# Kernel tuning notes

Measured on AMD Instinct MI355X. Metric: run time of the kernel, lower is better.

The kernel has to match this reference:

```python
import jax, jax.numpy as jnp
import numpy as np
import math

B, T, D = 4, 2048, 1024
H, DH = 16, 64  # n_heads, d_head; H*DH == D


def setup_inputs() -> dict:
    key = jax.random.key(0)
    ks = jax.random.split(key, 5)
    s = 0.02
    return {
        "x": jax.random.normal(ks[0], (B, T, D), dtype=jnp.float32),
        "W_qkv": jax.random.normal(ks[1], (D, 3 * D), dtype=jnp.float32) * s,
        "b_qkv": jnp.zeros((3 * D,), dtype=jnp.float32),
        "W_out": jax.random.normal(ks[2], (D, D), dtype=jnp.float32) * s,
        "b_out": jnp.zeros((D,), dtype=jnp.float32),
    }


def reference(x, W_qkv, b_qkv, W_out, b_out):
    Bx, Tx, Cx = x.shape
    qkv = x @ W_qkv + b_qkv                      # [B,T,3D]
    q, k, v = jnp.split(qkv, 3, axis=-1)
    q = q.reshape(Bx, Tx, H, DH).transpose(0, 2, 1, 3)  # [B,H,T,dh]
    k = k.reshape(Bx, Tx, H, DH).transpose(0, 2, 1, 3)
    v = v.reshape(Bx, Tx, H, DH).transpose(0, 2, 1, 3)
    scores = jnp.einsum("bhqd,bhkd->bhqk", q, k) / math.sqrt(DH)
    causal = jnp.tril(jnp.ones((Tx, Tx), dtype=bool))
    scores = jnp.where(causal, scores, jnp.float32(-jnp.inf))
    attn = jax.nn.softmax(scores, axis=-1)       # dropout p=0.0 -> identity
    out = jnp.einsum("bhqk,bhkd->bhqd", attn, v)
    out = out.transpose(0, 2, 1, 3).reshape(Bx, Tx, Cx)
    return out @ W_out + b_out
```

## Files before the change

### kernel.cpp

```cpp
#include <hip/hip_runtime.h>

#define DEVI __device__ __forceinline__

typedef __attribute__((ext_vector_type(8))) short short8;
typedef __attribute__((ext_vector_type(4))) float floatx4;

typedef const __attribute__((address_space(1))) void* gbl_ptr_t;
typedef __attribute__((address_space(3))) void* lds_ptr_t;

DEVI unsigned short f2bf(float f) {
  union { float f; unsigned int u; } v; v.f = f;
  unsigned int r = v.u + 0x7fffu + ((v.u >> 16) & 1u);
  return (unsigned short)(r >> 16);
}

DEVI float redsum16(float v) {
  v += __shfl_xor(v, 1);
  v += __shfl_xor(v, 2);
  v += __shfl_xor(v, 4);
  v += __shfl_xor(v, 8);
  return v;
}

constexpr int Bc = 4, Tc = 2048, Dc = 1024, Hc = 16, DHc = 64;
constexpr int Mrows = Bc * Tc;
constexpr long PLANE = (long)Bc * Hc * Tc * DHc;

__global__ __launch_bounds__(256) void cast_f32_bf16(const float* __restrict__ in,
                                                     unsigned short* __restrict__ out, int n4) {
  int i = blockIdx.x * 256 + threadIdx.x;
  if (i < n4) {
    float4 v = ((const float4*)in)[i];
    ushort4 o;
    o.x = f2bf(v.x); o.y = f2bf(v.y); o.z = f2bf(v.z); o.w = f2bf(v.w);
    ((ushort4*)out)[i] = o;
  }
}

__global__ __launch_bounds__(256) void transpose_cast(const float* __restrict__ in,
                                                      unsigned short* __restrict__ out,
                                                      int K, int N) {
  __shared__ float tile[32][33];
  int bx = blockIdx.x * 32;
  int by = blockIdx.y * 32;
  int tx = threadIdx.x & 31, ty = threadIdx.x >> 5;
#pragma unroll
  for (int i = ty; i < 32; i += 8) tile[i][tx] = in[(long)(by + i) * N + bx + tx];
  __syncthreads();
#pragma unroll
  for (int i = ty; i < 32; i += 8) out[(long)(bx + i) * K + by + tx] = f2bf(tile[tx][i]);
}

template <int MODE>
__global__ __launch_bounds__(256) void gemm_bt(const unsigned short* __restrict__ A,
                                               const unsigned short* __restrict__ Bt,
                                               const float* __restrict__ bias,
                                               void* __restrict__ Cout,
                                               int M, int N, int K) {
  constexpr int BK = 64;
  __shared__ __align__(16) short As[128 * 64];
  __shared__ __align__(16) short Bs[128 * 64];

  const int tid = threadIdx.x;
  const int wave = tid >> 6;
  const int lane = tid & 63;
  const int l16 = lane & 15;
  const int quad = lane >> 4;
  const int wm = (wave >> 1) * 64;
  const int wn = (wave & 1) * 64;
  const int rsub = lane >> 3;
  const int csub = (lane & 7) * 8;

  const long row0 = (long)blockIdx.y * 128;
  const long col0 = (long)blockIdx.x * 128;

  floatx4 acc[4][4];
#pragma unroll
  for (int i = 0; i < 4; i++)
#pragma unroll
    for (int j = 0; j < 4; j++) acc[i][j] = (floatx4){0.f, 0.f, 0.f, 0.f};

  for (int k0 = 0; k0 < K; k0 += BK) {
#pragma unroll
    for (int c = 0; c < 4; c++) {
      int rb = (c * 4 + wave) * 8;
      const unsigned short* sA = &A[(row0 + rb + rsub) * (long)K + k0 + csub];
      __builtin_amdgcn_global_load_lds((gbl_ptr_t)sA, (lds_ptr_t)&As[rb * 64], 16, 0, 0);
      const unsigned short* sB = &Bt[(col0 + rb + rsub) * (long)K + k0 + csub];
      __builtin_amdgcn_global_load_lds((gbl_ptr_t)sB, (lds_ptr_t)&Bs[rb * 64], 16, 0, 0);
    }
    __syncthreads();
#pragma unroll
    for (int kk = 0; kk < BK; kk += 32) {
      short8 af[4], bfr[4];
#pragma unroll
      for (int mt = 0; mt < 4; mt++)
        af[mt] = *(const short8*)&As[(wm + mt * 16 + l16) * 64 + kk + quad * 8];
#pragma unroll
      for (int nt = 0; nt < 4; nt++)
        bfr[nt] = *(const short8*)&Bs[(wn + nt * 16 + l16) * 64 + kk + quad * 8];
#pragma unroll
      for (int mt = 0; mt < 4; mt++)
#pragma unroll
        for (int nt = 0; nt < 4; nt++)
          acc[mt][nt] = __builtin_amdgcn_mfma_f32_16x16x32_bf16(af[mt], bfr[nt], acc[mt][nt], 0, 0, 0);
    }
    __syncthreads();
  }

#pragma unroll
  for (int mt = 0; mt < 4; mt++)
#pragma unroll
    for (int nt = 0; nt < 4; nt++)
#pragma unroll
      for (int r = 0; r < 4; r++) {
        long row = row0 + wm + mt * 16 + quad * 4 + r;
        long col = col0 + wn + nt * 16 + l16;
        float v = acc[mt][nt][r] + bias[col];
        if (MODE == 0) {
          int which = (int)(col >> 10);
          int hc = (int)col & 1023;
          int h = hc >> 6, d = hc & 63;
          int b = (int)(row >> 11), t = (int)row & 2047;
          ((unsigned short*)Cout)[(long)which * PLANE +
                                  (((long)(b * Hc + h) * Tc + t) << 6) + d] = f2bf(v);
        } else {
          ((float*)Cout)[row * N + col] = v;
        }
      }
}

__global__ __launch_bounds__(256) void flash_attn(const unsigned short* __restrict__ qkv,
                                                  unsigned short* __restrict__ attn_out) {
  constexpr int PD = 72;
  __shared__ __align__(16) short Ks[64 * PD];
  __shared__ __align__(16) short Vts[64 * PD];
  __shared__ __align__(16) short Ps[4 * 16 * PD];

  const int tid = threadIdx.x;
  const int wave = tid >> 6;
  const int lane = tid & 63;
  const int l16 = lane & 15;
  const int quad = lane >> 4;

  const int bh = blockIdx.y;
  const long base = (long)bh * Tc * DHc;
  const unsigned short* Qg = qkv + base;
  const unsigned short* Kg = qkv + PLANE + base;
  const unsigned short* Vg = qkv + 2 * PLANE + base;
  const int b = bh >> 4, h = bh & 15;

  constexpr float CEXP = 0.125f * 1.44269504f;
  short* Pw = &Ps[wave * 16 * PD];

  const int kr = tid >> 3;
  const int kc = (tid & 7) * 8;

#pragma unroll 1
  for (int pass = 0; pass < 2; pass++) {
    const int qx = (pass == 0) ? (int)blockIdx.x : (31 - (int)blockIdx.x);
    const int q0 = qx * 64 + wave * 16;

    short8 qf[2];
#pragma unroll
    for (int kk = 0; kk < 2; kk++)
      qf[kk] = *(const short8*)&Qg[(long)(q0 + l16) * 64 + kk * 32 + quad * 8];

    floatx4 oacc[4];
#pragma unroll
    for (int j = 0; j < 4; j++) oacc[j] = (floatx4){0.f, 0.f, 0.f, 0.f};
    float lpart[4] = {0.f, 0.f, 0.f, 0.f};

    const int ntiles = qx + 1;

    uint4 Kreg[2], Vreg[2];
    Kreg[0] = *(const uint4*)&Kg[(long)kr * 64 + kc];
    Kreg[1] = *(const uint4*)&Kg[(long)(32 + kr) * 64 + kc];
    Vreg[0] = *(const uint4*)&Vg[(long)lane * 64 + wave * 8];
    Vreg[1] = *(const uint4*)&Vg[(long)lane * 64 + (wave + 4) * 8];

#pragma unroll 1
    for (int kt = 0; kt < ntiles; kt++) {
      __syncthreads();
      *(uint4*)&Ks[kr * PD + kc] = Kreg[0];
      *(uint4*)&Ks[(32 + kr) * PD + kc] = Kreg[1];
#pragma unroll
      for (int c = 0; c < 2; c++) {
        int dc = wave + 4 * c;
        unsigned short vb[8];
        *(uint4*)vb = Vreg[c];
#pragma unroll
        for (int j = 0; j < 8; j++) Vts[(dc * 8 + j) * PD + lane] = (short)vb[j];
      }
      __syncthreads();
      if (kt + 1 < ntiles) {
        long koff = (long)(kt + 1) * 64;
        Kreg[0] = *(const uint4*)&Kg[(koff + kr) * 64 + kc];
        Kreg[1] = *(const uint4*)&Kg[(koff + 32 + kr) * 64 + kc];
        Vreg[0] = *(const uint4*)&Vg[(koff + lane) * 64 + wave * 8];
        Vreg[1] = *(const uint4*)&Vg[(koff + lane) * 64 + (wave + 4) * 8];
      }

      floatx4 sacc[4];
#pragma unroll
      for (int j = 0; j < 4; j++) sacc[j] = (floatx4){0.f, 0.f, 0.f, 0.f};
#pragma unroll
      for (int kk = 0; kk < 2; kk++) {
        short8 kf[4];
#pragma unroll
        for (int nt = 0; nt < 4; nt++)
          kf[nt] = *(const short8*)&Ks[(nt * 16 + l16) * PD + kk * 32 + quad * 8];
#pragma unroll
        for (int nt = 0; nt < 4; nt++)
          sacc[nt] = __builtin_amdgcn_mfma_f32_16x16x32_bf16(qf[kk], kf[nt], sacc[nt], 0, 0, 0);
      }

      if (kt == qx) {
#pragma unroll
        for (int nt = 0; nt < 4; nt++) {
          int ki = kt * 64 + nt * 16 + l16;
#pragma unroll
          for (int r = 0; r < 4; r++) {
            int qi = q0 + quad * 4 + r;
            if (ki > qi) sacc[nt][r] = -3.0e38f;
          }
        }
      }

#pragma unroll
      for (int nt = 0; nt < 4; nt++)
#pragma unroll
        for (int r = 0; r < 4; r++) sacc[nt][r] = exp2f(sacc[nt][r] * CEXP);
#pragma unroll
      for (int r = 0; r < 4; r++)
        lpart[r] += (sacc[0][r] + sacc[1][r]) + (sacc[2][r] + sacc[3][r]);

#pragma unroll
      for (int nt = 0; nt < 4; nt++)
#pragma unroll
        for (int r = 0; r < 4; r++)
          Pw[(quad * 4 + r) * PD + nt * 16 + l16] = (short)f2bf(sacc[nt][r]);

#pragma unroll
      for (int kk = 0; kk < 2; kk++) {
        short8 pf = *(const short8*)&Pw[l16 * PD + kk * 32 + quad * 8];
        short8 vf[4];
#pragma unroll
        for (int dt = 0; dt < 4; dt++)
          vf[dt] = *(const short8*)&Vts[(dt * 16 + l16) * PD + kk * 32 + quad * 8];
#pragma unroll
        for (int dt = 0; dt < 4; dt++)
          oacc[dt] = __builtin_amdgcn_mfma_f32_16x16x32_bf16(pf, vf[dt], oacc[dt], 0, 0, 0);
      }
    }

#pragma unroll
    for (int r = 0; r < 4; r++) {
      float l = redsum16(lpart[r]);
      float inv = 1.0f / l;
      int t = q0 + quad * 4 + r;
#pragma unroll
      for (int dt = 0; dt < 4; dt++) {
        int d = dt * 16 + l16;
        attn_out[(((long)(b * Tc + t) * Hc + h) << 6) + d] = f2bf(oacc[dt][r] * inv);
      }
    }
  }
}

extern "C" void kernel_launch(void* const* d_in, const int* in_sizes, int n_in,
                              void* d_out, int out_size, void* d_ws, size_t ws_size,
                              hipStream_t stream) {
  const float* x = (const float*)d_in[0];
  const float* Wqkv = (const float*)d_in[1];
  const float* bqkv = (const float*)d_in[2];
  const float* Wout = (const float*)d_in[3];
  const float* bout = (const float*)d_in[4];

  char* ws = (char*)d_ws;
  unsigned short* x_bf   = (unsigned short*)ws;
  unsigned short* wqkv_t = (unsigned short*)(ws + 16777216);
  unsigned short* wout_t = (unsigned short*)(ws + 16777216 + 6291456);
  unsigned short* qkv    = (unsigned short*)(ws + 25165824);
  unsigned short* attn   = x_bf;

  cast_f32_bf16<<<dim3(Mrows * Dc / 4 / 256), dim3(256), 0, stream>>>(x, x_bf, Mrows * Dc / 4);
  transpose_cast<<<dim3(3 * Dc / 32, Dc / 32), dim3(256), 0, stream>>>(Wqkv, wqkv_t, Dc, 3 * Dc);
  transpose_cast<<<dim3(Dc / 32, Dc / 32), dim3(256), 0, stream>>>(Wout, wout_t, Dc, Dc);

  gemm_bt<0><<<dim3(3 * Dc / 128, Mrows / 128), dim3(256), 0, stream>>>(
      x_bf, wqkv_t, bqkv, qkv, Mrows, 3 * Dc, Dc);

  flash_attn<<<dim3(16, Bc * Hc), dim3(256), 0, stream>>>(qkv, attn);

  gemm_bt<1><<<dim3(Dc / 128, Mrows / 128), dim3(256), 0, stream>>>(
      attn, wout_t, bout, d_out, Mrows, Dc, Dc);
}
```

Measured before the change: 324.5 us.

## Store V transposed from QKV GEMM and compute transposed scores in attention

The QKV GEMM epilogue now writes V in a [bh][d][t] layout, so the attention kernel can stage V into LDS with vector stores instead of a scalar transpose. The QK MFMA operands are swapped to produce S^T, which lets each lane pack P into 8-byte LDS stores and compute the row sum with fewer shuffles. The LDS row pad is changed to 80, and the grid is reordered so blocks for the same query tile across heads are scheduled together. The risk is that the transposed V writes in the GEMM epilogue are strided by T, so they are poorly coalesced and may slow that kernel.

Measured after the change: 386.6 us. 19.1% more time.

```diff
diff --git a/kernel.cpp b/kernel.cpp
--- a/kernel.cpp
+++ b/kernel.cpp
@@ -12,14 +12,6 @@
   union { float f; unsigned int u; } v; v.f = f;
   unsigned int r = v.u + 0x7fffu + ((v.u >> 16) & 1u);
   return (unsigned short)(r >> 16);
-}
-
-DEVI float redsum16(float v) {
-  v += __shfl_xor(v, 1);
-  v += __shfl_xor(v, 2);
-  v += __shfl_xor(v, 4);
-  v += __shfl_xor(v, 8);
-  return v;
 }
 
 constexpr int Bc = 4, Tc = 2048, Dc = 1024, Hc = 16, DHc = 64;
@@ -122,8 +114,12 @@
           int hc = (int)col & 1023;
           int h = hc >> 6, d = hc & 63;
           int b = (int)(row >> 11), t = (int)row & 2047;
-          ((unsigned short*)Cout)[(long)which * PLANE +
-                                  (((long)(b * Hc + h) * Tc + t) << 6) + d] = f2bf(v);
+          long bh = b * Hc + h;
+          if (which == 2) {
+            ((unsigned short*)Cout)[2 * PLANE + bh * (64L * Tc) + (long)d * Tc + t] = f2bf(v);
+          } else {
+            ((unsigned short*)Cout)[(long)which * PLANE + ((bh * Tc + t) << 6) + d] = f2bf(v);
+          }
         } else {
           ((float*)Cout)[row * N + col] = v;
         }
@@ -132,7 +128,7 @@
 
 __global__ __launch_bounds__(256) void flash_attn(const unsigned short* __restrict__ qkv,
                                                   unsigned short* __restrict__ attn_out) {
-  constexpr int PD = 72;
+  constexpr int PD = 80;
   __shared__ __align__(16) short Ks[64 * PD];
   __shared__ __align__(16) short Vts[64 * PD];
   __shared__ __align__(16) short Ps[4 * 16 * PD];
@@ -143,11 +139,10 @@
   const int l16 = lane & 15;
   const int quad = lane >> 4;
 
-  const int bh = blockIdx.y;
-  const long base = (long)bh * Tc * DHc;
-  const unsigned short* Qg = qkv + base;
-  const unsigned short* Kg = qkv + PLANE + base;
-  const unsigned short* Vg = qkv + 2 * PLANE + base;
+  const int bh = blockIdx.x;
+  const unsigned short* Qg = qkv + (long)bh * Tc * DHc;
+  const unsigned short* Kg = qkv + PLANE + (long)bh * Tc * DHc;
+  const unsigned short* VgT = qkv + 2 * PLANE + (long)bh * (64L * Tc);
   const int b = bh >> 4, h = bh & 15;
 
   constexpr float CEXP = 0.125f * 1.44269504f;
@@ -158,7 +153,7 @@
 
 #pragma unroll 1
   for (int pass = 0; pass < 2; pass++) {
-    const int qx = (pass == 0) ? (int)blockIdx.x : (31 - (int)blockIdx.x);
+    const int qx = (pass == 0) ? (int)blockIdx.y : (31 - (int)blockIdx.y);
     const int q0 = qx * 64 + wave * 16;
 
     short8 qf[2];
@@ -169,36 +164,30 @@
     floatx4 oacc[4];
 #pragma unroll
     for (int j = 0; j < 4; j++) oacc[j] = (floatx4){0.f, 0.f, 0.f, 0.f};
-    float lpart[4] = {0.f, 0.f, 0.f, 0.f};
+    float lp = 0.f;
 
     const int ntiles = qx + 1;
 
     uint4 Kreg[2], Vreg[2];
     Kreg[0] = *(const uint4*)&Kg[(long)kr * 64 + kc];
     Kreg[1] = *(const uint4*)&Kg[(long)(32 + kr) * 64 + kc];
-    Vreg[0] = *(const uint4*)&Vg[(long)lane * 64 + wave * 8];
-    Vreg[1] = *(const uint4*)&Vg[(long)lane * 64 + (wave + 4) * 8];
+    Vreg[0] = *(const uint4*)&VgT[(long)kr * Tc + kc];
+    Vreg[1] = *(const uint4*)&VgT[(long)(32 + kr) * Tc + kc];
 
 #pragma unroll 1
     for (int kt = 0; kt < ntiles; kt++) {
       __syncthreads();
       *(uint4*)&Ks[kr * PD + kc] = Kreg[0];
       *(uint4*)&Ks[(32 + kr) * PD + kc] = Kreg[1];
-#pragma unroll
-      for (int c = 0; c < 2; c++) {
-        int dc = wave + 4 * c;
-        unsigned short vb[8];
-        *(uint4*)vb = Vreg[c];
-#pragma unroll
-        for (int j = 0; j < 8; j++) Vts[(dc * 8 + j) * PD + lane] = (short)vb[j];
-      }
+      *(uint4*)&Vts[kr * PD + kc] = Vreg[0];
+      *(uint4*)&Vts[(32 + kr) * PD + kc] = Vreg[1];
       __syncthreads();
       if (kt + 1 < ntiles) {
         long koff = (long)(kt + 1) * 64;
         Kreg[0] = *(const uint4*)&Kg[(koff + kr) * 64 + kc];
         Kreg[1] = *(const uint4*)&Kg[(koff + 32 + kr) * 64 + kc];
-        Vreg[0] = *(const uint4*)&Vg[(koff + lane) * 64 + wave * 8];
-        Vreg[1] = *(const uint4*)&Vg[(koff + lane) * 64 + (wave + 4) * 8];
+        Vreg[0] = *(const uint4*)&VgT[(long)kr * Tc + koff + kc];
+        Vreg[1] = *(const uint4*)&VgT[(long)(32 + kr) * Tc + koff + kc];
       }
 
       floatx4 sacc[4];
@@ -212,18 +201,17 @@
           kf[nt] = *(const short8*)&Ks[(nt * 16 + l16) * PD + kk * 32 + quad * 8];
 #pragma unroll
         for (int nt = 0; nt < 4; nt++)
-          sacc[nt] = __builtin_amdgcn_mfma_f32_16x16x32_bf16(qf[kk], kf[nt], sacc[nt], 0, 0, 0);
+          sacc[nt] = __builtin_amdgcn_mfma_f32_16x16x32_bf16(kf[nt], qf[kk], sacc[nt], 0, 0, 0);
       }
 
       if (kt == qx) {
+        int qi = q0 + l16;
 #pragma unroll
         for (int nt = 0; nt < 4; nt++) {
-          int ki = kt * 64 + nt * 16 + l16;
-#pragma unroll
-          for (int r = 0; r < 4; r++) {
-            int qi = q0 + quad * 4 + r;
-            if (ki > qi) sacc[nt][r] = -3.0e38f;
-          }
+          int kbase = kt * 64 + nt * 16 + quad * 4;
+#pragma unroll
+          for (int r = 0; r < 4; r++)
+            if (kbase + r > qi) sacc[nt][r] = -3.0e38f;
         }
       }
 
@@ -232,14 +220,16 @@
 #pragma unroll
         for (int r = 0; r < 4; r++) sacc[nt][r] = exp2f(sacc[nt][r] * CEXP);
 #pragma unroll
-      for (int r = 0; r < 4; r++)
-        lpart[r] += (sacc[0][r] + sacc[1][r]) + (sacc[2][r] + sacc[3][r]);
-
-#pragma unroll
       for (int nt = 0; nt < 4; nt++)
-#pragma unroll
-        for (int r = 0; r < 4; r++)
-          Pw[(quad * 4 + r) * PD + nt * 16 + l16] = (short)f2bf(sacc[nt][r]);
+        lp += (sacc[nt][0] + sacc[nt][1]) + (sacc[nt][2] + sacc[nt][3]);
+
+#pragma unroll
+      for (int nt = 0; nt < 4; nt++) {
+        unsigned int u0 = (unsigned int)f2bf(sacc[nt][0]) | ((unsigned int)f2bf(sacc[nt][1]) << 16);
+        unsigned int u1 = (unsigned int)f2bf(sacc[nt][2]) | ((unsigned int)f2bf(sacc[nt][3]) << 16);
+        uint2 u = {u0, u1};
+        *(uint2*)&Pw[l16 * PD + nt * 16 + quad * 4] = u;
+      }
 
 #pragma unroll
       for (int kk = 0; kk < 2; kk++) {
@@ -254,10 +244,12 @@
       }
     }
 
+    float lv = lp + __shfl_xor(lp, 16);
+    lv += __shfl_xor(lv, 32);
 #pragma unroll
     for (int r = 0; r < 4; r++) {
-      float l = redsum16(lpart[r]);
-      float inv = 1.0f / l;
+      float lr = __shfl(lv, quad * 4 + r);
+      float inv = 1.0f / lr;
       int t = q0 + quad * 4 + r;
 #pragma unroll
       for (int dt = 0; dt < 4; dt++) {
@@ -291,7 +283,7 @@
   gemm_bt<0><<<dim3(3 * Dc / 128, Mrows / 128), dim3(256), 0, stream>>>(
       x_bf, wqkv_t, bqkv, qkv, Mrows, 3 * Dc, Dc);
 
-  flash_attn<<<dim3(16, Bc * Hc), dim3(256), 0, stream>>>(qkv, attn);
+  flash_attn<<<dim3(Bc * Hc, 16), dim3(256), 0, stream>>>(qkv, attn);
 
   gemm_bt<1><<<dim3(Dc / 128, Mrows / 128), dim3(256), 0, stream>>>(
       attn, wout_t, bout, d_out, Mrows, Dc, Dc);
```
